# Kernel optimization log

Hardware: AMD Instinct MI355X
Metric: run time of the kernel (lower is better)

The kernel has to match this reference:

```python
import jax, jax.numpy as jnp
import numpy as np

IN_DIM, D_MODEL, HIDDEN, N_BLOCKS, N_CLASSES = 784, 16, 6, 4, 10
BATCH = 65536


def setup_inputs() -> dict:
    key = jax.random.key(0)
    ks = jax.random.split(key, 6)
    std = 0.02
    x = jax.random.normal(ks[0], (BATCH, IN_DIM), dtype=jnp.float32)
    # nn.Linear stores weight as [out, in]; we keep that convention.
    W_embed = jax.random.normal(ks[1], (D_MODEL, IN_DIM), dtype=jnp.float32) * std
    L_w = jax.random.normal(ks[2], (N_BLOCKS, HIDDEN, D_MODEL), dtype=jnp.float32) * std
    R_w = jax.random.normal(ks[3], (N_BLOCKS, HIDDEN, D_MODEL), dtype=jnp.float32) * std
    D_w = jax.random.normal(ks[4], (N_BLOCKS, D_MODEL, HIDDEN), dtype=jnp.float32) * std
    W_head = jax.random.normal(ks[5], (N_CLASSES, D_MODEL), dtype=jnp.float32) * std
    return {"x": x, "W_embed": W_embed, "L_w": L_w, "R_w": R_w, "D_w": D_w, "W_head": W_head}


def reference(x, W_embed, L_w, R_w, D_w, W_head):
    # embed: [B, in_dim] @ [in_dim, d_model]
    h_x = x @ W_embed.T  # [B, d_model]
    all_h = []
    for i in range(N_BLOCKS):  # n_blocks is a small structural constant
        u = h_x @ L_w[i].T  # [B, hidden]
        v = h_x @ R_w[i].T  # [B, hidden]
        h = u * v
        h_x = h_x + h @ D_w[i].T  # residual
        all_h.append(h)
    logits = h_x @ W_head.T  # [B, n_classes]
    return (logits, *all_h)
```

## Files before the change

### kernel.cpp

```cpp
#include <hip/hip_runtime.h>


#define IN_DIM   784
#define D_MODEL  16
#define HIDDEN   6
#define N_BLOCKS 4
#define N_CLS    10
#define BATCH    65536
#define NCHUNK   12

typedef const __attribute__((address_space(1))) void gvoid_t;
typedef __attribute__((address_space(3))) void svoid_t;

__global__ __launch_bounds__(256, 4) void bilinear_resnet_fused(
    const float* __restrict__ x,
    const float* __restrict__ W_embed,
    const float* __restrict__ L_w,
    const float* __restrict__ R_w,
    const float* __restrict__ D_w,
    const float* __restrict__ W_head,
    float* __restrict__ out)
{
    __shared__ float4 buf[2][64 * 16];

    const int tid  = threadIdx.x;
    const int lane = tid & 63;
    const int wv   = __builtin_amdgcn_readfirstlane(tid >> 6);
    const int row  = blockIdx.x * 64 + lane;
    const float* xtile = x + (size_t)blockIdx.x * 64 * IN_DIM;

    const int sub   = lane >> 4;
    const int rmod  = wv * 4 + sub;
    const int kk_l  = (lane & 15) ^ rmod;

    float acc[D_MODEL];
#pragma unroll
    for (int d = 0; d < D_MODEL; ++d) acc[d] = 0.f;

#pragma unroll
    for (int it = 0; it < 4; ++it) {
        const int r = it * 16 + rmod;
        const float* g = xtile + (size_t)r * IN_DIM + kk_l * 4;
        char* l = (char*)(&buf[0][0]) + (it * 256 + wv * 64) * 16;
        __builtin_amdgcn_global_load_lds((gvoid_t*)g, (svoid_t*)l, 16, 0, 0);
    }
    __syncthreads();

    for (int c = 0; c < NCHUNK; ++c) {
        if (c + 1 < NCHUNK) {
#pragma unroll
            for (int it = 0; it < 4; ++it) {
                const int r = it * 16 + rmod;
                const float* g = xtile + (size_t)r * IN_DIM + (c + 1) * 64 + kk_l * 4;
                char* l = (char*)(&buf[(c + 1) & 1][0]) + (it * 256 + wv * 64) * 16;
                __builtin_amdgcn_global_load_lds((gvoid_t*)g, (svoid_t*)l, 16, 0, 0);
            }
        }
        const float* wc = W_embed + c * 64 + wv * 16;
        const float4* bsrc = buf[c & 1];
#pragma unroll
        for (int j = 0; j < 4; ++j) {
            const int kk = wv * 4 + j;
            const float4 xv = bsrc[lane * 16 + (kk ^ (lane & 15))];
#pragma unroll
            for (int d = 0; d < D_MODEL; ++d) {
                const float* wd = wc + d * IN_DIM + j * 4;
                float s = acc[d];
                s = fmaf(xv.x, wd[0], s);
                s = fmaf(xv.y, wd[1], s);
                s = fmaf(xv.z, wd[2], s);
                s = fmaf(xv.w, wd[3], s);
                acc[d] = s;
            }
        }
        __syncthreads();
    }

    {
        const float4 xv = *reinterpret_cast<const float4*>(
            x + (size_t)row * IN_DIM + 768 + wv * 4);
        const float* wt = W_embed + 768 + wv * 4;
#pragma unroll
        for (int d = 0; d < D_MODEL; ++d) {
            const float* wd = wt + d * IN_DIM;
            float s = acc[d];
            s = fmaf(xv.x, wd[0], s);
            s = fmaf(xv.y, wd[1], s);
            s = fmaf(xv.z, wd[2], s);
            s = fmaf(xv.w, wd[3], s);
            acc[d] = s;
        }
    }

    float* parts = reinterpret_cast<float*>(&buf[0][0]);
    if (wv != 0) {
#pragma unroll
        for (int d = 0; d < D_MODEL; ++d)
            parts[((wv - 1) * 64 + lane) * 17 + d] = acc[d];
    }
    __syncthreads();
    if (wv != 0) return;

#pragma unroll
    for (int d = 0; d < D_MODEL; ++d)
        acc[d] += parts[(0 * 64 + lane) * 17 + d]
                + parts[(1 * 64 + lane) * 17 + d]
                + parts[(2 * 64 + lane) * 17 + d];

#pragma unroll
    for (int b = 0; b < N_BLOCKS; ++b) {
        const float* Lb = L_w + b * HIDDEN * D_MODEL;
        const float* Rb = R_w + b * HIDDEN * D_MODEL;
        const float* Db = D_w + b * D_MODEL * HIDDEN;
        float h[HIDDEN];
#pragma unroll
        for (int j = 0; j < HIDDEN; ++j) {
            float u = 0.f, v = 0.f;
#pragma unroll
            for (int d = 0; d < D_MODEL; ++d) {
                u = fmaf(acc[d], Lb[j * D_MODEL + d], u);
                v = fmaf(acc[d], Rb[j * D_MODEL + d], v);
            }
            h[j] = u * v;
        }
#pragma unroll
        for (int d = 0; d < D_MODEL; ++d) {
            float s = acc[d];
#pragma unroll
            for (int j = 0; j < HIDDEN; ++j) s = fmaf(h[j], Db[d * HIDDEN + j], s);
            acc[d] = s;
        }
        float* hout = out + (size_t)N_CLS * BATCH + (size_t)b * HIDDEN * BATCH
                      + (size_t)row * HIDDEN;
#pragma unroll
        for (int j = 0; j < HIDDEN; ++j) hout[j] = h[j];
    }

    float* lout = out + (size_t)row * N_CLS;
#pragma unroll
    for (int k = 0; k < N_CLS; ++k) {
        float s = 0.f;
#pragma unroll
        for (int d = 0; d < D_MODEL; ++d) s = fmaf(acc[d], W_head[k * D_MODEL + d], s);
        lout[k] = s;
    }
}

extern "C" void kernel_launch(void* const* d_in, const int* in_sizes, int n_in,
                              void* d_out, int out_size, void* d_ws, size_t ws_size,
                              hipStream_t stream) {
    const float* x       = (const float*)d_in[0];
    const float* W_embed = (const float*)d_in[1];
    const float* L_w     = (const float*)d_in[2];
    const float* R_w     = (const float*)d_in[3];
    const float* D_w     = (const float*)d_in[4];
    const float* W_head  = (const float*)d_in[5];
    float* out = (float*)d_out;

    const int grid = BATCH / 64;
    bilinear_resnet_fused<<<grid, 256, 0, stream>>>(
        x, W_embed, L_w, R_w, D_w, W_head, out);
}
```

Baseline: 334.3 us.

## Triple-buffer x tile staging with manual vmcnt waits and barriers

Replaces the double-buffered LDS staging of x chunks with a three-slot ring, so two chunks of global-to-LDS loads stay in flight while one chunk is computed. Full __syncthreads are replaced by explicit s_waitcnt vmcnt counts plus s_barrier, which allows partial waits on outstanding loads. LDS use grows by half and the occupancy hint drops from 4 to 3 blocks per CU. The hand-counted waits also rely on the exact number of outstanding memory operations, which makes them fragile.

```diff
diff --git a/kernel.cpp b/kernel.cpp
--- a/kernel.cpp
+++ b/kernel.cpp
@@ -12,7 +12,7 @@
 typedef const __attribute__((address_space(1))) void gvoid_t;
 typedef __attribute__((address_space(3))) void svoid_t;
 
-__global__ __launch_bounds__(256, 4) void bilinear_resnet_fused(
+__global__ __launch_bounds__(256, 3) void bilinear_resnet_fused(
     const float* __restrict__ x,
     const float* __restrict__ W_embed,
     const float* __restrict__ L_w,
@@ -21,7 +21,7 @@
     const float* __restrict__ W_head,
     float* __restrict__ out)
 {
-    __shared__ float4 buf[2][64 * 16];
+    __shared__ float4 buf[3][64 * 16];
 
     const int tid  = threadIdx.x;
     const int lane = tid & 63;
@@ -37,27 +37,19 @@
 #pragma unroll
     for (int d = 0; d < D_MODEL; ++d) acc[d] = 0.f;
 
+    auto stage = [&](int k, int slot) {
 #pragma unroll
-    for (int it = 0; it < 4; ++it) {
-        const int r = it * 16 + rmod;
-        const float* g = xtile + (size_t)r * IN_DIM + kk_l * 4;
-        char* l = (char*)(&buf[0][0]) + (it * 256 + wv * 64) * 16;
-        __builtin_amdgcn_global_load_lds((gvoid_t*)g, (svoid_t*)l, 16, 0, 0);
-    }
-    __syncthreads();
+        for (int it = 0; it < 4; ++it) {
+            const int r = it * 16 + rmod;
+            const float* g = xtile + (size_t)r * IN_DIM + k * 64 + kk_l * 4;
+            char* l = (char*)(&buf[slot][0]) + (it * 256 + wv * 64) * 16;
+            __builtin_amdgcn_global_load_lds((gvoid_t*)g, (svoid_t*)l, 16, 0, 0);
+        }
+    };
 
-    for (int c = 0; c < NCHUNK; ++c) {
-        if (c + 1 < NCHUNK) {
-#pragma unroll
-            for (int it = 0; it < 4; ++it) {
-                const int r = it * 16 + rmod;
-                const float* g = xtile + (size_t)r * IN_DIM + (c + 1) * 64 + kk_l * 4;
-                char* l = (char*)(&buf[(c + 1) & 1][0]) + (it * 256 + wv * 64) * 16;
-                __builtin_amdgcn_global_load_lds((gvoid_t*)g, (svoid_t*)l, 16, 0, 0);
-            }
-        }
+    auto compute = [&](int c, int slot) {
         const float* wc = W_embed + c * 64 + wv * 16;
-        const float4* bsrc = buf[c & 1];
+        const float4* bsrc = buf[slot];
 #pragma unroll
         for (int j = 0; j < 4; ++j) {
             const int kk = wv * 4 + j;
@@ -73,8 +65,38 @@
                 acc[d] = s;
             }
         }
-        __syncthreads();
+    };
+
+    stage(0, 0);
+    stage(1, 1);
+    stage(2, 2);
+    asm volatile("s_waitcnt vmcnt(8)" ::: "memory");
+    __builtin_amdgcn_s_barrier();
+    asm volatile("" ::: "memory");
+
+#pragma unroll 3
+    for (int c = 0; c < NCHUNK - 3; ++c) {
+        compute(c, c % 3);
+        asm volatile("s_waitcnt lgkmcnt(0)" ::: "memory");
+        __builtin_amdgcn_s_barrier();
+        asm volatile("" ::: "memory");
+        stage(c + 3, c % 3);
+        asm volatile("s_waitcnt vmcnt(8)" ::: "memory");
+        __builtin_amdgcn_s_barrier();
+        asm volatile("" ::: "memory");
     }
+
+    compute(9, 0);
+    asm volatile("s_waitcnt vmcnt(4)" ::: "memory");
+    __builtin_amdgcn_s_barrier();
+    asm volatile("" ::: "memory");
+
+    compute(10, 1);
+    asm volatile("s_waitcnt vmcnt(0)" ::: "memory");
+    __builtin_amdgcn_s_barrier();
+    asm volatile("" ::: "memory");
+
+    compute(11, 2);
 
     {
         const float4 xv = *reinterpret_cast<const float4*>(
```

After: 389.0 us. 1.16x slower.

## Split the embedding K-reduction across eight waves per 512-thread block

Applied to the files above, without the earlier changes.

Blocks grow from 256 to 512 threads, so eight waves share each 64-row tile instead of four. Each wave now covers 8 of the 64 columns per chunk and 2 of the 16 tail columns. The staging loop is rewritten so 512 threads fill the swizzled LDS buffer in two passes. The tail load is hoisted to the start of the kernel, and wave 0 now reduces seven partial sums instead of three. The aim is more memory-level parallelism and more waves in flight to hide load latency. In exchange, the tighter launch bounds cap registers per thread and the cross-wave reduction gets longer.

```diff
diff --git a/kernel.cpp b/kernel.cpp
--- a/kernel.cpp
+++ b/kernel.cpp
@@ -12,7 +12,7 @@
 typedef const __attribute__((address_space(1))) void gvoid_t;
 typedef __attribute__((address_space(3))) void svoid_t;
 
-__global__ __launch_bounds__(256, 4) void bilinear_resnet_fused(
+__global__ __launch_bounds__(512, 8) void bilinear_resnet_fused(
     const float* __restrict__ x,
     const float* __restrict__ W_embed,
     const float* __restrict__ L_w,
@@ -29,38 +29,32 @@
     const int row  = blockIdx.x * 64 + lane;
     const float* xtile = x + (size_t)blockIdx.x * 64 * IN_DIM;
 
-    const int sub   = lane >> 4;
-    const int rmod  = wv * 4 + sub;
-    const int kk_l  = (lane & 15) ^ rmod;
+    const int rhalf = tid >> 4;
+    const int kk_l  = (tid & 15) ^ (rhalf & 15);
+
+    const float2 xtail = *reinterpret_cast<const float2*>(
+        x + (size_t)row * IN_DIM + 768 + wv * 2);
 
     float acc[D_MODEL];
 #pragma unroll
     for (int d = 0; d < D_MODEL; ++d) acc[d] = 0.f;
 
+    auto stage = [&](int k, int b) {
 #pragma unroll
-    for (int it = 0; it < 4; ++it) {
-        const int r = it * 16 + rmod;
-        const float* g = xtile + (size_t)r * IN_DIM + kk_l * 4;
-        char* l = (char*)(&buf[0][0]) + (it * 256 + wv * 64) * 16;
-        __builtin_amdgcn_global_load_lds((gvoid_t*)g, (svoid_t*)l, 16, 0, 0);
-    }
-    __syncthreads();
+        for (int it = 0; it < 2; ++it) {
+            const int r = it * 32 + rhalf;
+            const float* g = xtile + (size_t)r * IN_DIM + k * 64 + kk_l * 4;
+            char* l = (char*)(&buf[b][0]) + (it * 512 + tid) * 16;
+            __builtin_amdgcn_global_load_lds((gvoid_t*)g, (svoid_t*)l, 16, 0, 0);
+        }
+    };
 
-    for (int c = 0; c < NCHUNK; ++c) {
-        if (c + 1 < NCHUNK) {
+    auto compute = [&](int c, int b) {
+        const float* wc = W_embed + c * 64 + wv * 8;
+        const float4* bsrc = buf[b];
 #pragma unroll
-            for (int it = 0; it < 4; ++it) {
-                const int r = it * 16 + rmod;
-                const float* g = xtile + (size_t)r * IN_DIM + (c + 1) * 64 + kk_l * 4;
-                char* l = (char*)(&buf[(c + 1) & 1][0]) + (it * 256 + wv * 64) * 16;
-                __builtin_amdgcn_global_load_lds((gvoid_t*)g, (svoid_t*)l, 16, 0, 0);
-            }
-        }
-        const float* wc = W_embed + c * 64 + wv * 16;
-        const float4* bsrc = buf[c & 1];
-#pragma unroll
-        for (int j = 0; j < 4; ++j) {
-            const int kk = wv * 4 + j;
+        for (int j = 0; j < 2; ++j) {
+            const int kk = wv * 2 + j;
             const float4 xv = bsrc[lane * 16 + (kk ^ (lane & 15))];
 #pragma unroll
             for (int d = 0; d < D_MODEL; ++d) {
@@ -73,22 +67,23 @@
                 acc[d] = s;
             }
         }
+    };
+
+    stage(0, 0);
+    __syncthreads();
+
+    for (int c = 0; c < NCHUNK; ++c) {
+        if (c + 1 < NCHUNK) stage(c + 1, (c + 1) & 1);
+        compute(c, c & 1);
         __syncthreads();
     }
 
     {
-        const float4 xv = *reinterpret_cast<const float4*>(
-            x + (size_t)row * IN_DIM + 768 + wv * 4);
-        const float* wt = W_embed + 768 + wv * 4;
+        const float* wt = W_embed + 768 + wv * 2;
 #pragma unroll
         for (int d = 0; d < D_MODEL; ++d) {
             const float* wd = wt + d * IN_DIM;
-            float s = acc[d];
-            s = fmaf(xv.x, wd[0], s);
-            s = fmaf(xv.y, wd[1], s);
-            s = fmaf(xv.z, wd[2], s);
-            s = fmaf(xv.w, wd[3], s);
-            acc[d] = s;
+            acc[d] = fmaf(xtail.x, wd[0], fmaf(xtail.y, wd[1], acc[d]));
         }
     }
 
@@ -102,10 +97,10 @@
     if (wv != 0) return;
 
 #pragma unroll
-    for (int d = 0; d < D_MODEL; ++d)
-        acc[d] += parts[(0 * 64 + lane) * 17 + d]
-                + parts[(1 * 64 + lane) * 17 + d]
-                + parts[(2 * 64 + lane) * 17 + d];
+    for (int p = 0; p < 7; ++p)
+#pragma unroll
+        for (int d = 0; d < D_MODEL; ++d)
+            acc[d] += parts[(p * 64 + lane) * 17 + d];
 
 #pragma unroll
     for (int b = 0; b < N_BLOCKS; ++b) {
@@ -158,6 +153,6 @@
     float* out = (float*)d_out;
 
     const int grid = BATCH / 64;
-    bilinear_resnet_fused<<<grid, 256, 0, stream>>>(
+    bilinear_resnet_fused<<<grid, 512, 0, stream>>>(
         x, W_embed, L_w, R_w, D_w, W_head, out);
 }
```

Measured after the change: 329.5 us. About the same (-1.4%).
